# Kernel optimization log

Measured on AMD Instinct MI355X. Metric: run time of the kernel, lower is better.

Reference implementation:

```python
import jax, jax.numpy as jnp
import numpy as np

B, S, D, H = 2, 2048, 1024, 16
DK = D // H  # 64
EPS = 1e-5


def setup_inputs() -> dict:
    key = jax.random.key(0)
    ks = jax.random.split(key, 12)
    sc = 1.0 / np.sqrt(D)
    inp = {
        "Q": jax.random.normal(ks[0], (B, S, D), jnp.float32),
        "K": jax.random.normal(ks[1], (B, S, D), jnp.float32),
        "V": jax.random.normal(ks[2], (B, S, D), jnp.float32),
        # causal mask: True = masked out
        "attn_mask": jnp.broadcast_to(jnp.triu(jnp.ones((S, S), bool), k=1), (B, S, S)),
        # torch Linear weights stored [out, in]
        "Wq": jax.random.normal(ks[3], (D, D), jnp.float32) * sc,
        "bq": jnp.zeros((D,), jnp.float32),
        "Wk": jax.random.normal(ks[4], (D, D), jnp.float32) * sc,
        "bk": jnp.zeros((D,), jnp.float32),
        "Wv": jax.random.normal(ks[5], (D, D), jnp.float32) * sc,
        "bv": jnp.zeros((D,), jnp.float32),
        "Wo": jax.random.normal(ks[6], (D, D), jnp.float32) * sc,
        "bo": jnp.zeros((D,), jnp.float32),
        "gamma": jnp.ones((D,), jnp.float32),
        "beta": jnp.zeros((D,), jnp.float32),
    }
    return inp


def _layer_norm(x, gamma, beta):
    mu = jnp.mean(x, axis=-1, keepdims=True)
    var = jnp.mean(jnp.square(x - mu), axis=-1, keepdims=True)
    return (x - mu) * jax.lax.rsqrt(var + EPS) * gamma + beta


def reference(Q, K, V, attn_mask, Wq, bq, Wk, bk, Wv, bv, Wo, bo, gamma, beta):
    residual = Q
    # projections -> [B, H, S, DK]
    q = (Q @ Wq.T + bq).reshape(B, S, H, DK).transpose(0, 2, 1, 3)
    k = (K @ Wk.T + bk).reshape(B, S, H, DK).transpose(0, 2, 1, 3)
    v = (V @ Wv.T + bv).reshape(B, S, H, DK).transpose(0, 2, 1, 3)
    scores = jnp.einsum("bhqd,bhkd->bhqk", q, k) / np.sqrt(DK)
    scores = jnp.where(attn_mask[:, None, :, :], -1e9, scores)
    attn = jax.nn.softmax(scores, axis=-1)
    ctx = jnp.einsum("bhqk,bhkd->bhqd", attn, v)  # [B,H,S,DK]
    ctx = ctx.transpose(0, 2, 1, 3).reshape(B, S, H * DK)
    out = ctx @ Wo.T + bo
    return _layer_norm(out + residual, gamma, beta), attn
```

## Files before the change

### kernel.cpp

```cpp
#include <hip/hip_runtime.h>
#include <hip/hip_fp16.h>

#define BB 2
#define SS 2048
#define DD 1024
#define HH 16
#define DKK 64
#define BHH (BB*HH)
#define MM (BB*SS)
#define EPSF 1e-5f

typedef _Float16 f16;
typedef _Float16 f16x4 __attribute__((ext_vector_type(4)));
typedef _Float16 f16x8 __attribute__((ext_vector_type(8)));
typedef float f32x4 __attribute__((ext_vector_type(4)));

__device__ __forceinline__ int swz128(int row, int byteInRow) {
    return row * 128 + (byteInRow ^ ((row & 7) << 4));
}

__device__ __forceinline__ void gl_lds16(const f16* g, f16* l) {
    __builtin_amdgcn_global_load_lds((const __attribute__((address_space(1))) void*)g,
                                     (__attribute__((address_space(3))) void*)l, 16, 0, 0);
}

__global__ __launch_bounds__(256) void cvt_pass(
    const float* __restrict__ s0, const float* __restrict__ s1, const float* __restrict__ s2,
    const float* __restrict__ s3, const float* __restrict__ s4, const float* __restrict__ s5,
    const float* __restrict__ s6,
    f16* __restrict__ d0, f16* __restrict__ d1, f16* __restrict__ d2,
    f16* __restrict__ d3, f16* __restrict__ d4, f16* __restrict__ d5, f16* __restrict__ d6)
{
    const int y = blockIdx.y;
    const float* s; f16* d; int n4;
    switch (y) {
        case 0: s = s0; d = d0; n4 = (MM * DD) / 4; break;
        case 1: s = s1; d = d1; n4 = (MM * DD) / 4; break;
        case 2: s = s2; d = d2; n4 = (MM * DD) / 4; break;
        case 3: s = s3; d = d3; n4 = (DD * DD) / 4; break;
        case 4: s = s4; d = d4; n4 = (DD * DD) / 4; break;
        case 5: s = s5; d = d5; n4 = (DD * DD) / 4; break;
        default: s = s6; d = d6; n4 = (DD * DD) / 4; break;
    }
    for (int i = blockIdx.x * 256 + threadIdx.x; i < n4; i += 256 * 256) {
        f32x4 v = ((const f32x4*)s)[i];
        f16x4 h = { (f16)v.x, (f16)v.y, (f16)v.z, (f16)v.w };
        ((f16x4*)d)[i] = h;
    }
}

__global__ __launch_bounds__(256) void qkv_gemm(
    const f16* __restrict__ Qf, const f16* __restrict__ Kf, const f16* __restrict__ Vf,
    const f16* __restrict__ Wqf, const float* __restrict__ bq,
    const f16* __restrict__ Wkf, const float* __restrict__ bk,
    const f16* __restrict__ Wvf, const float* __restrict__ bv,
    f16* __restrict__ qh, f16* __restrict__ kh, f16* __restrict__ vTh)
{
    const int type = blockIdx.z;
    const f16* X = (type == 0) ? Qf : (type == 1) ? Kf : Vf;
    const f16* W = (type == 0) ? Wqf : (type == 1) ? Wkf : Wvf;
    const float* bias = (type == 0) ? bq : (type == 1) ? bk : bv;
    const int m0 = blockIdx.y * 128, n0 = blockIdx.x * 128;

    __shared__ f16 smem[2][128 * 64];
    f16* a_lds = smem[0];
    f16* b_lds = smem[1];

    const int t = threadIdx.x;
    const int l = t & 63, w = t >> 6;
    const int wr = (w >> 1) * 64, wc = (w & 1) * 64;

    f32x4 acc[4][4] = {};

    for (int k0 = 0; k0 < DD; k0 += 64) {
        __syncthreads();
        #pragma unroll
        for (int p = 0; p < 4; p++) {
            int idx = w * 4 + p;
            int gci = idx * 64 + l;
            int row = gci >> 3, slot = gci & 7;
            int ss = slot ^ (row & 7);
            gl_lds16(X + (size_t)(m0 + row) * DD + k0 + ss * 8, a_lds + idx * 512);
            gl_lds16(W + (size_t)(n0 + row) * DD + k0 + ss * 8, b_lds + idx * 512);
        }
        __syncthreads();
        #pragma unroll
        for (int kk = 0; kk < 2; kk++) {
            f16x8 af[4], bf[4];
            #pragma unroll
            for (int mi = 0; mi < 4; mi++) {
                int row = wr + mi * 16 + (l & 15);
                af[mi] = *(const f16x8*)((const char*)a_lds + swz128(row, kk * 64 + (l >> 4) * 16));
            }
            #pragma unroll
            for (int ni = 0; ni < 4; ni++) {
                int row = wc + ni * 16 + (l & 15);
                bf[ni] = *(const f16x8*)((const char*)b_lds + swz128(row, kk * 64 + (l >> 4) * 16));
            }
            #pragma unroll
            for (int mi = 0; mi < 4; mi++)
                #pragma unroll
                for (int ni = 0; ni < 4; ni++)
                    acc[mi][ni] = __builtin_amdgcn_mfma_f32_16x16x32_f16(af[mi], bf[ni], acc[mi][ni], 0, 0, 0);
        }
    }

    if (type == 2) {
        __syncthreads();
        f16* tb = smem[0];
        #pragma unroll
        for (int mi = 0; mi < 4; mi++) {
            #pragma unroll
            for (int ni = 0; ni < 4; ni++) {
                int nl = wc + ni * 16 + (l & 15);
                int mb = (wr + mi * 16 + (l >> 4) * 4) * 2;
                f16x4 hv;
                #pragma unroll
                for (int r = 0; r < 4; r++)
                    hv[r] = (f16)(acc[mi][ni][r] + bias[n0 + nl]);
                *(f16x4*)((char*)tb + nl * 256 + (mb ^ ((nl & 7) << 4))) = hv;
            }
        }
        __syncthreads();
        const int b = m0 >> 11;
        const int mloc = m0 & (SS - 1);
        #pragma unroll
        for (int i = 0; i < 8; i++) {
            int o = w * 8192 + i * 1024 + l * 16;
            int nl = o >> 8;
            int inb = o & 255;
            f16x8 v = *(const f16x8*)((char*)tb + nl * 256 + (inb ^ ((nl & 7) << 4)));
            int ng = n0 + nl, h_ = ng >> 6, dk = ng & 63;
            int s = mloc + inb / 2;
            *(f16x8*)(vTh + ((size_t)((b * HH + h_) * DKK + dk)) * SS + s) = v;
        }
    } else {
        #pragma unroll
        for (int mi = 0; mi < 4; mi++) {
            #pragma unroll
            for (int ni = 0; ni < 4; ni++) {
                #pragma unroll
                for (int r = 0; r < 4; r++) {
                    int m = m0 + wr + mi * 16 + (l >> 4) * 4 + r;
                    int n = n0 + wc + ni * 16 + (l & 15);
                    float v = acc[mi][ni][r] + bias[n];
                    f16 hv = (f16)v;
                    int b = m >> 11, s = m & (SS - 1);
                    int h_ = n >> 6, dk = n & (DKK - 1);
                    f16* dst = (type == 0) ? qh : kh;
                    dst[((size_t)((b * HH + h_) * SS + s)) * DKK + dk] = hv;
                }
            }
        }
    }
}

__global__ __launch_bounds__(256) void attn_kernel(
    const f16* __restrict__ qh, const f16* __restrict__ kh, const f16* __restrict__ vTh,
    float* __restrict__ attn_out, f16* __restrict__ ctx)
{
    const int bid = blockIdx.x;
    const int swz = (bid & 7) * 128 + (bid >> 3);
    const int bh = swz >> 5;
    const int qb = 31 - (swz & 31);
    const int qbase = qb * 64;
    const int t = threadIdx.x, l = t & 63, w = t >> 6;
    const int c = l & 15, g = l >> 4;

    __shared__ f16 kb[2][64 * 64];
    __shared__ f16 vb[2][64 * 64];

    const float CSC = 0.125f * 1.44269504f;
    const int nj = qb + 1;
    const int qloc = w * 16 + c;
    const int qglob = qbase + qloc;

    const f16* kbase = kh + (size_t)bh * SS * DKK;
    const f16* vbase = vTh + (size_t)bh * DKK * SS;
    float* aout = attn_out + (size_t)bh * SS * SS;

    const f16* qsrc = qh + (size_t)bh * SS * DKK + (size_t)qglob * DKK;
    f16x8 bq[2];
    bq[0] = *(const f16x8*)(qsrc + g * 8);
    bq[1] = *(const f16x8*)(qsrc + 32 + g * 8);

    #define STAGE_K(jt, buf) { \
        const f16* ksrc_ = kbase + (size_t)(jt) * 64 * DKK; \
        _Pragma("unroll") \
        for (int p = 0; p < 2; p++) { \
            int idx = w * 2 + p; \
            int gci = idx * 64 + l; \
            int row = gci >> 3, slot = gci & 7; \
            int ss_ = slot ^ (row & 7); \
            gl_lds16(ksrc_ + row * DKK + ss_ * 8, kb[buf] + idx * 512); \
        } }
    #define STAGE_V(jt, buf) { \
        const f16* vsrc_ = vbase + (size_t)(jt) * 64; \
        _Pragma("unroll") \
        for (int p = 0; p < 2; p++) { \
            int idx = w * 2 + p; \
            int gci = idx * 64 + l; \
            int row = gci >> 3, slot = gci & 7; \
            int ss_ = slot ^ (row & 7); \
            gl_lds16(vsrc_ + (size_t)row * SS + ss_ * 8, vb[buf] + idx * 512); \
        } }

    #define QKT(dstf, srcb) { \
        __builtin_amdgcn_s_setprio(1); \
        _Pragma("unroll") \
        for (int dw = 0; dw < 2; dw++) { \
            _Pragma("unroll") \
            for (int ni = 0; ni < 4; ni++) { \
                f16x8 ak = *(const f16x8*)((const char*)(srcb) + swz128(ni * 16 + c, dw * 64 + g * 16)); \
                dstf[ni] = __builtin_amdgcn_mfma_f32_16x16x32_f16(ak, bq[dw], dstf[ni], 0, 0, 0); \
            } \
        } \
        __builtin_amdgcn_s_setprio(0); }

    #define PSTORE(jt) { \
        float* pl_ = (float*)vb; \
        _Pragma("unroll") \
        for (int i = 0; i < 4; i++) { \
            int row_ = w * 16 + 4 * i + g; \
            f32x4 v_ = *(const f32x4*)((char*)pl_ + row_ * 256 + ((c * 16) ^ ((row_ & 7) << 4))); \
            __builtin_nontemporal_store(v_, (f32x4*)(aout + (size_t)(qbase + row_) * SS + (jt) * 64 + c * 4)); \
        } }

    STAGE_K(0, 0);
    __syncthreads();

    float lrow = 0.f;
    f32x4 cacc[4] = {};
    f32x4 sprev[4];

    for (int j = 0; j < nj; j++) {
        if (j + 1 < nj) STAGE_K(j + 1, (j + 1) & 1);
        STAGE_V(j, j & 1);

        f32x4 scur[4] = {};
        QKT(scur, kb[j & 1]);

        if (j > 0) {
            const f16* pvv = vb[(j - 1) & 1];
            f16x4 bfr[4];
            #pragma unroll
            for (int ni = 0; ni < 4; ni++) {
                float e0 = exp2f(sprev[ni][0] * CSC);
                float e1 = exp2f(sprev[ni][1] * CSC);
                float e2 = exp2f(sprev[ni][2] * CSC);
                float e3 = exp2f(sprev[ni][3] * CSC);
                lrow += e0 + e1 + e2 + e3;
                bfr[ni] = f16x4{ (f16)e0, (f16)e1, (f16)e2, (f16)e3 };
            }
            __builtin_amdgcn_s_setprio(1);
            #pragma unroll
            for (int ni2 = 0; ni2 < 4; ni2++) {
                #pragma unroll
                for (int nk = 0; nk < 4; nk++) {
                    f16x4 av = *(const f16x4*)((const char*)pvv + swz128(ni2 * 16 + c, nk * 32 + g * 8));
                    cacc[ni2] = __builtin_amdgcn_mfma_f32_16x16x16f16(av, bfr[nk], cacc[ni2], 0, 0, 0);
                }
            }
            __builtin_amdgcn_s_setprio(0);
        }
        __syncthreads();
        #pragma unroll
        for (int x = 0; x < 4; x++) sprev[x] = scur[x];
    }

    STAGE_K(0, 0);

    {
        const f16* pvv = vb[(nj - 1) & 1];
        f16x4 bfr[4];
        #pragma unroll
        for (int ni = 0; ni < 4; ni++) {
            int kkb = ni * 16 + 4 * g;
            float e0 = (kkb + 0 > qloc) ? 0.f : exp2f(sprev[ni][0] * CSC);
            float e1 = (kkb + 1 > qloc) ? 0.f : exp2f(sprev[ni][1] * CSC);
            float e2 = (kkb + 2 > qloc) ? 0.f : exp2f(sprev[ni][2] * CSC);
            float e3 = (kkb + 3 > qloc) ? 0.f : exp2f(sprev[ni][3] * CSC);
            lrow += e0 + e1 + e2 + e3;
            bfr[ni] = f16x4{ (f16)e0, (f16)e1, (f16)e2, (f16)e3 };
        }
        __builtin_amdgcn_s_setprio(1);
        #pragma unroll
        for (int ni2 = 0; ni2 < 4; ni2++) {
            #pragma unroll
            for (int nk = 0; nk < 4; nk++) {
                f16x4 av = *(const f16x4*)((const char*)pvv + swz128(ni2 * 16 + c, nk * 32 + g * 8));
                cacc[ni2] = __builtin_amdgcn_mfma_f32_16x16x16f16(av, bfr[nk], cacc[ni2], 0, 0, 0);
            }
        }
        __builtin_amdgcn_s_setprio(0);
    }

    lrow += __shfl_xor(lrow, 16);
    lrow += __shfl_xor(lrow, 32);
    const float rinv = 1.f / lrow;
    const float nls = -__log2f(lrow);

    {
        int b = bh >> 4, h_ = bh & 15;
        f16* cbase = ctx + (size_t)(b * SS + qglob) * DD + h_ * 64;
        #pragma unroll
        for (int ni2 = 0; ni2 < 4; ni2++) {
            f16x4 hv = { (f16)(cacc[ni2][0] * rinv), (f16)(cacc[ni2][1] * rinv),
                         (f16)(cacc[ni2][2] * rinv), (f16)(cacc[ni2][3] * rinv) };
            *(f16x4*)(cbase + ni2 * 16 + 4 * g) = hv;
        }
    }

    __syncthreads();

    {
        float* pl = (float*)vb;
        for (int j = 0; j < nj; j++) {
            if (j + 1 < nj) STAGE_K(j + 1, (j + 1) & 1);

            f32x4 scur[4] = {};
            QKT(scur, kb[j & 1]);

            if (j > 0) {
                #pragma unroll
                for (int ni = 0; ni < 4; ni++) {
                    f32x4 st = { exp2f(fmaf(sprev[ni][0], CSC, nls)),
                                 exp2f(fmaf(sprev[ni][1], CSC, nls)),
                                 exp2f(fmaf(sprev[ni][2], CSC, nls)),
                                 exp2f(fmaf(sprev[ni][3], CSC, nls)) };
                    *(f32x4*)((char*)pl + (w * 16 + c) * 256 + ((ni * 64 + g * 16) ^ ((c & 7) << 4))) = st;
                }
                PSTORE(j - 1);
            }
            __syncthreads();
            #pragma unroll
            for (int x = 0; x < 4; x++) sprev[x] = scur[x];
        }

        {
            #pragma unroll
            for (int ni = 0; ni < 4; ni++) {
                int kkb = ni * 16 + 4 * g;
                f32x4 st = { (kkb + 0 > qloc) ? 0.f : exp2f(fmaf(sprev[ni][0], CSC, nls)),
                             (kkb + 1 > qloc) ? 0.f : exp2f(fmaf(sprev[ni][1], CSC, nls)),
                             (kkb + 2 > qloc) ? 0.f : exp2f(fmaf(sprev[ni][2], CSC, nls)),
                             (kkb + 3 > qloc) ? 0.f : exp2f(fmaf(sprev[ni][3], CSC, nls)) };
                *(f32x4*)((char*)pl + (w * 16 + c) * 256 + ((ni * 64 + g * 16) ^ ((c & 7) << 4))) = st;
            }
            PSTORE(nj - 1);
        }
    }

    {
        f32x4 z = { 0.f, 0.f, 0.f, 0.f };
        for (int jb = qb + 1; jb < 32; jb++) {
            #pragma unroll
            for (int i = 0; i < 4; i++) {
                int c2 = t + 256 * i;
                int row = c2 >> 4, cg = c2 & 15;
                __builtin_nontemporal_store(z, (f32x4*)(aout + (size_t)(qbase + row) * SS + jb * 64 + cg * 4));
            }
        }
    }
    #undef STAGE_K
    #undef STAGE_V
    #undef QKT
    #undef PSTORE
}

__global__ __launch_bounds__(256) void oproj_gemm(
    const f16* __restrict__ A, const f16* __restrict__ Wof, const float* __restrict__ bo,
    const float* __restrict__ resid, float* __restrict__ out)
{
    const int m0 = blockIdx.y * 128, n0 = blockIdx.x * 128;
    __shared__ f16 a_lds[128 * 64];
    __shared__ f16 b_lds[128 * 64];
    const int t = threadIdx.x;
    const int l = t & 63, w = t >> 6;
    const int wr = (w >> 1) * 64, wc = (w & 1) * 64;

    f32x4 acc[4][4] = {};

    for (int k0 = 0; k0 < DD; k0 += 64) {
        __syncthreads();
        #pragma unroll
        for (int p = 0; p < 4; p++) {
            int idx = w * 4 + p;
            int gci = idx * 64 + l;
            int row = gci >> 3, slot = gci & 7;
            int ss = slot ^ (row & 7);
            gl_lds16(A + (size_t)(m0 + row) * DD + k0 + ss * 8, a_lds + idx * 512);
            gl_lds16(Wof + (size_t)(n0 + row) * DD + k0 + ss * 8, b_lds + idx * 512);
        }
        __syncthreads();
        #pragma unroll
        for (int kk = 0; kk < 2; kk++) {
            f16x8 af[4], bf[4];
            #pragma unroll
            for (int mi = 0; mi < 4; mi++) {
                int row = wr + mi * 16 + (l & 15);
                af[mi] = *(const f16x8*)((const char*)a_lds + swz128(row, kk * 64 + (l >> 4) * 16));
            }
            #pragma unroll
            for (int ni = 0; ni < 4; ni++) {
                int row = wc + ni * 16 + (l & 15);
                bf[ni] = *(const f16x8*)((const char*)b_lds + swz128(row, kk * 64 + (l >> 4) * 16));
            }
            #pragma unroll
            for (int mi = 0; mi < 4; mi++)
                #pragma unroll
                for (int ni = 0; ni < 4; ni++)
                    acc[mi][ni] = __builtin_amdgcn_mfma_f32_16x16x32_f16(af[mi], bf[ni], acc[mi][ni], 0, 0, 0);
        }
    }

    #pragma unroll
    for (int mi = 0; mi < 4; mi++) {
        #pragma unroll
        for (int ni = 0; ni < 4; ni++) {
            #pragma unroll
            for (int r = 0; r < 4; r++) {
                int m = m0 + wr + mi * 16 + (l >> 4) * 4 + r;
                int n = n0 + wc + ni * 16 + (l & 15);
                float v = acc[mi][ni][r] + bo[n] + resid[(size_t)m * DD + n];
                out[(size_t)m * DD + n] = v;
            }
        }
    }
}

__global__ __launch_bounds__(256) void ln_kernel(
    const float* __restrict__ x, const float* __restrict__ gamma,
    const float* __restrict__ beta, float* __restrict__ out)
{
    int row = blockIdx.x;
    int t = threadIdx.x;
    float4 v = ((const float4*)(x + (size_t)row * DD))[t];
    float s = v.x + v.y + v.z + v.w;
    __shared__ float red[4];
    #pragma unroll
    for (int o = 32; o; o >>= 1) s += __shfl_down(s, o, 64);
    if ((t & 63) == 0) red[t >> 6] = s;
    __syncthreads();
    float mean = (red[0] + red[1] + red[2] + red[3]) * (1.f / DD);
    __syncthreads();
    float4 d;
    d.x = v.x - mean; d.y = v.y - mean; d.z = v.z - mean; d.w = v.w - mean;
    float q = d.x * d.x + d.y * d.y + d.z * d.z + d.w * d.w;
    #pragma unroll
    for (int o = 32; o; o >>= 1) q += __shfl_down(q, o, 64);
    if ((t & 63) == 0) red[t >> 6] = q;
    __syncthreads();
    float var = (red[0] + red[1] + red[2] + red[3]) * (1.f / DD);
    float rstd = rsqrtf(var + EPSF);
    float4 g = ((const float4*)gamma)[t];
    float4 bt = ((const float4*)beta)[t];
    float4 o4;
    o4.x = d.x * rstd * g.x + bt.x;
    o4.y = d.y * rstd * g.y + bt.y;
    o4.z = d.z * rstd * g.z + bt.z;
    o4.w = d.w * rstd * g.w + bt.w;
    ((float4*)(out + (size_t)row * DD))[t] = o4;
}

extern "C" void kernel_launch(void* const* d_in, const int* in_sizes, int n_in,
                              void* d_out, int out_size, void* d_ws, size_t ws_size,
                              hipStream_t stream)
{
    const float* Q     = (const float*)d_in[0];
    const float* K     = (const float*)d_in[1];
    const float* V     = (const float*)d_in[2];
    const float* Wq    = (const float*)d_in[4];
    const float* bq    = (const float*)d_in[5];
    const float* Wk    = (const float*)d_in[6];
    const float* bk    = (const float*)d_in[7];
    const float* Wv    = (const float*)d_in[8];
    const float* bv    = (const float*)d_in[9];
    const float* Wo    = (const float*)d_in[10];
    const float* bo    = (const float*)d_in[11];
    const float* gamma = (const float*)d_in[12];
    const float* beta  = (const float*)d_in[13];

    float* out_ln   = (float*)d_out;
    float* attn_out = (float*)d_out + (size_t)BB * SS * DD;

    f16* Qf  = (f16*)attn_out;
    f16* Kf  = Qf + (size_t)MM * DD;
    f16* Vf  = Kf + (size_t)MM * DD;
    f16* Wqf = (f16*)out_ln;
    f16* Wkf = Wqf + (size_t)DD * DD;
    f16* Wvf = Wkf + (size_t)DD * DD;
    f16* Wof = Wvf + (size_t)DD * DD;

    char* ws = (char*)d_ws;
    f16*   qh    = (f16*)(ws);
    f16*   kh    = (f16*)(ws + ((size_t)8  << 20));
    f16*   vTh   = (f16*)(ws + ((size_t)16 << 20));
    f16*   ctx   = (f16*)(ws + ((size_t)24 << 20));
    float* oproj = (float*)(ws + ((size_t)32 << 20));

    cvt_pass<<<dim3(256, 7), 256, 0, stream>>>(Q, K, V, Wq, Wk, Wv, Wo,
                                               Qf, Kf, Vf, Wqf, Wkf, Wvf, Wof);
    qkv_gemm<<<dim3(8, 32, 3), 256, 0, stream>>>(Qf, Kf, Vf, Wqf, bq, Wkf, bk, Wvf, bv, qh, kh, vTh);
    attn_kernel<<<dim3(1024), 256, 0, stream>>>(qh, kh, vTh, attn_out, ctx);
    oproj_gemm<<<dim3(8, 32), 256, 0, stream>>>(ctx, Wof, bo, Q, oproj);
    ln_kernel<<<dim3(MM), 256, 0, stream>>>(oproj, gamma, beta, out_ln);
}
```

Measured before the change: 234.0 us.

## Triple-buffer K/V tiles in attention with partial vmcnt waits

Moves the attention kernel's K and V LDS staging from double to triple buffering. K is prefetched two tiles ahead and V one tile ahead, and each __syncthreads is replaced with an explicit s_waitcnt vmcnt(n) plus s_barrier. This lets loads for later tiles stay in flight across the barrier instead of draining all outstanding memory operations each iteration. The cost is higher LDS use (48KB vs 32KB), which can lower occupancy, plus hand-tuned vmcnt counts that must match the issued loads and nontemporal stores exactly.

```diff
diff --git a/kernel.cpp b/kernel.cpp
--- a/kernel.cpp
+++ b/kernel.cpp
@@ -167,8 +167,8 @@
     const int t = threadIdx.x, l = t & 63, w = t >> 6;
     const int c = l & 15, g = l >> 4;
 
-    __shared__ f16 kb[2][64 * 64];
-    __shared__ f16 vb[2][64 * 64];
+    __shared__ f16 kb3[3][64 * 64];
+    __shared__ f16 vb3[3][64 * 64];
 
     const float CSC = 0.125f * 1.44269504f;
     const int nj = qb + 1;
@@ -192,7 +192,7 @@
             int gci = idx * 64 + l; \
             int row = gci >> 3, slot = gci & 7; \
             int ss_ = slot ^ (row & 7); \
-            gl_lds16(ksrc_ + row * DKK + ss_ * 8, kb[buf] + idx * 512); \
+            gl_lds16(ksrc_ + row * DKK + ss_ * 8, kb3[buf] + idx * 512); \
         } }
     #define STAGE_V(jt, buf) { \
         const f16* vsrc_ = vbase + (size_t)(jt) * 64; \
@@ -202,7 +202,7 @@
             int gci = idx * 64 + l; \
             int row = gci >> 3, slot = gci & 7; \
             int ss_ = slot ^ (row & 7); \
-            gl_lds16(vsrc_ + (size_t)row * SS + ss_ * 8, vb[buf] + idx * 512); \
+            gl_lds16(vsrc_ + (size_t)row * SS + ss_ * 8, vb3[buf] + idx * 512); \
         } }
 
     #define QKT(dstf, srcb) { \
@@ -218,7 +218,7 @@
         __builtin_amdgcn_s_setprio(0); }
 
     #define PSTORE(jt) { \
-        float* pl_ = (float*)vb; \
+        float* pl_ = (float*)vb3; \
         _Pragma("unroll") \
         for (int i = 0; i < 4; i++) { \
             int row_ = w * 16 + 4 * i + g; \
@@ -226,22 +226,28 @@
             __builtin_nontemporal_store(v_, (f32x4*)(aout + (size_t)(qbase + row_) * SS + (jt) * 64 + c * 4)); \
         } }
 
+    #define CBAR(n) { asm volatile("s_waitcnt vmcnt(" #n ")"); \
+                      __builtin_amdgcn_s_barrier(); \
+                      __builtin_amdgcn_sched_barrier(0); }
+
     STAGE_K(0, 0);
-    __syncthreads();
+    if (nj > 1) STAGE_K(1, 1);
+    STAGE_V(0, 0);
+    CBAR(0);
 
     float lrow = 0.f;
     f32x4 cacc[4] = {};
     f32x4 sprev[4];
 
     for (int j = 0; j < nj; j++) {
-        if (j + 1 < nj) STAGE_K(j + 1, (j + 1) & 1);
-        STAGE_V(j, j & 1);
+        if (j + 2 < nj) STAGE_K(j + 2, (j + 2) % 3);
+        if (j + 1 < nj) STAGE_V(j + 1, (j + 1) % 3);
 
         f32x4 scur[4] = {};
-        QKT(scur, kb[j & 1]);
+        QKT(scur, kb3[j % 3]);
 
         if (j > 0) {
-            const f16* pvv = vb[(j - 1) & 1];
+            const f16* pvv = vb3[(j - 1) % 3];
             f16x4 bfr[4];
             #pragma unroll
             for (int ni = 0; ni < 4; ni++) {
@@ -263,15 +269,20 @@
             }
             __builtin_amdgcn_s_setprio(0);
         }
-        __syncthreads();
+
+        if (j + 3 <= nj)      CBAR(4)
+        else if (j + 2 == nj) CBAR(2)
+        else                  CBAR(0);
+
         #pragma unroll
         for (int x = 0; x < 4; x++) sprev[x] = scur[x];
     }
 
     STAGE_K(0, 0);
+    if (nj > 1) STAGE_K(1, 1);
 
     {
-        const f16* pvv = vb[(nj - 1) & 1];
+        const f16* pvv = vb3[(nj - 1) % 3];
         f16x4 bfr[4];
         #pragma unroll
         for (int ni = 0; ni < 4; ni++) {
@@ -311,15 +322,15 @@
         }
     }
 
-    __syncthreads();
+    CBAR(0);
 
     {
-        float* pl = (float*)vb;
+        float* pl = (float*)vb3;
         for (int j = 0; j < nj; j++) {
-            if (j + 1 < nj) STAGE_K(j + 1, (j + 1) & 1);
+            if (j + 2 < nj) STAGE_K(j + 2, (j + 2) % 3);
 
             f32x4 scur[4] = {};
-            QKT(scur, kb[j & 1]);
+            QKT(scur, kb3[j % 3]);
 
             if (j > 0) {
                 #pragma unroll
@@ -332,7 +343,12 @@
                 }
                 PSTORE(j - 1);
             }
-            __syncthreads();
+
+            if (j == 0 && j + 2 < nj)  CBAR(2)
+            else if (j + 2 < nj)       CBAR(6)
+            else if (j > 0)            CBAR(4)
+            else                       CBAR(0);
+
             #pragma unroll
             for (int x = 0; x < 4; x++) sprev[x] = scur[x];
         }
@@ -366,6 +382,7 @@
     #undef STAGE_V
     #undef QKT
     #undef PSTORE
+    #undef CBAR
 }
 
 __global__ __launch_bounds__(256) void oproj_gemm(
```

Result: faster. 219.8 us (-6.1%).
